# Optimization experiments

Hardware: AMD Instinct MI355X
Metric: run time of the kernel (lower is better)

Reference implementation:

```python
import jax, jax.numpy as jnp
import numpy as np

N_CLASSES = 12
IMG_SIZE = 512
BATCH = 8

CURV_MAX = jnp.array([1.2261, 1.1558, 1.1161, 1.1195, 2.7202, 2.3714,
                      1.7055, 3.2717, 2.6716, 5.0418, 0.4293], dtype=jnp.float32)


def setup_inputs() -> dict:
    key = jax.random.key(0)
    soft_anatomy = jax.random.normal(key, (BATCH, N_CLASSES, IMG_SIZE, IMG_SIZE), dtype=jnp.float32)
    return {"soft_anatomy": soft_anatomy}


def reference(soft_anatomy):
    nc1 = N_CLASSES - 1  # 11 layer channels
    pred_mask = soft_anatomy[:, :nc1]                      # [B, 11, H, W]
    sm = jax.nn.softmax(pred_mask, axis=2)                 # softmax over height (dim 2)
    lsm = jax.nn.log_softmax(pred_mask, axis=2)
    B, C, H, W = sm.shape

    # position mask: row index broadcast over width/channels
    pos = jnp.arange(H, dtype=sm.dtype)[None, None, :, None]  # [1,1,H,1]

    # expected layer position per column: [B, 11, W]
    layer_positions = jnp.sum(sm * pos, axis=2)

    # std deviations around layer positions: [B, 11, W]
    std_deviations = jnp.sqrt(
        jnp.sum(sm * (pos - layer_positions[:, :, None, :]) ** 2, axis=2))

    # topology violations between adjacent layers: [B, 10, W]
    topology_violations = jax.nn.relu(layer_positions[:, :-1] - layer_positions[:, 1:])

    # neighbour (continuity) diff along width: [B, 11, W-1]
    continuity_violations = jnp.abs(
        (jnp.roll(layer_positions, 1, axis=2) - layer_positions)[..., 1:])

    # curvature via depthwise conv1d with sobel [-1,0..0,1] and laplace [1,0..0,-2,0..0,1]
    # (kernel length 11, replicate pad 5 -> same width). torch conv1d is cross-correlation:
    #   first[w]  = -x[w] + x[w+10]
    #   second[w] =  x[w] - 2*x[w+5] + x[w+10]
    PAD = 5
    lpp = jnp.pad(layer_positions, ((0, 0), (0, 0), (PAD, PAD)), mode='edge')
    first_order = lpp[..., 10:] - lpp[..., :-10]
    second_order = lpp[..., :-10] - 2.0 * lpp[..., 5:-5] + lpp[..., 10:]
    curvature = second_order / jnp.power(1.0 + first_order ** 2, 1.5)
    curvature_diffs = jnp.abs(curvature) - CURV_MAX[None, :, None]  # curv_max broadcast over W

    # topological_engine_1d: new[i] = max(new[i-1], lp[i]) == cumulative max over class dim
    correct_layer_positions = jax.lax.cummax(layer_positions, axis=1)

    # cumulative mask: ones channel + cumsum over height -> [B, 12, H, W]
    cum = jnp.cumsum(sm, axis=2)
    ones = jnp.ones((B, 1, H, W), dtype=sm.dtype)
    cm = jnp.concatenate([ones, cum], axis=1)

    # topological_engine_2d: y[idx] = relu(c[idx] + y[idx-1] - 1), idx = 2..n_classes-1
    def step(carry, c):
        y = jax.nn.relu(c + carry - 1.0)
        return y, y

    _, ys = jax.lax.scan(step, cm[:, 1], jnp.moveaxis(cm[:, 2:], 1, 0))
    top_correct = jnp.concatenate([cm[:, :2], jnp.moveaxis(ys, 0, 1)], axis=1)  # [B,12,H,W]

    # separate_masks: forward diff in place; last channel unchanged
    clean_masks = jnp.concatenate(
        [top_correct[:, :-1] - top_correct[:, 1:], top_correct[:, -1:]], axis=1)

    return (lsm, correct_layer_positions, clean_masks,
            std_deviations, topology_violations, continuity_violations, curvature_diffs)
```

## Files before the change

kernel.cpp:

```cpp
#include <hip/hip_runtime.h>

#define BB 8
#define NC 12
#define NC1 11
#define HH 512
#define WW 512
#define NCH 32
#define HC 16
#define NBC (BB*NC1)

static constexpr size_t CH_STRIDE = (size_t)HH * WW;

static constexpr size_t OFF_LSM   = 0;
static constexpr size_t OFF_CLP   = 23068672;
static constexpr size_t OFF_CLEAN = 23113728;
static constexpr size_t OFF_STD   = 48279552;
static constexpr size_t OFF_TOPO  = 48324608;
static constexpr size_t OFF_CONT  = 48365568;
static constexpr size_t OFF_CURV  = 48410536;

static constexpr size_t WS_E    = 0;
static constexpr size_t WS_P    = (size_t)NBC * NCH * WW;
static constexpr size_t WS_Q    = 2 * WS_P;
static constexpr size_t WS_INVS = 3 * WS_P;
static constexpr size_t WS_LOGS = WS_INVS + (size_t)NBC * WW;
static constexpr size_t WS_LP   = WS_LOGS + (size_t)NBC * WW;

__global__ __launch_bounds__(512) void k1_partials(const float* __restrict__ in,
                                                   float* __restrict__ ws) {
    const int w = threadIdx.x;
    const int chunk = blockIdx.x;
    const int bc = blockIdx.y;
    const int b = bc / NC1, c = bc % NC1;

    const float* p = in + ((size_t)(b * NC + c) * HH + (size_t)chunk * HC) * WW + w;
    float E = 0.f, P = 0.f, Q = 0.f;
#pragma unroll
    for (int i = 0; i < HC; ++i) {
        float x = p[(size_t)i * WW];
        float e = expf(x);
        float h = (float)(chunk * HC + i);
        E += e;
        P += h * e;
        Q += h * h * e;
    }
    size_t o = ((size_t)bc * NCH + chunk) * WW + w;
    ws[WS_E + o] = E;
    ws[WS_P + o] = P;
    ws[WS_Q + o] = Q;
}

__global__ __launch_bounds__(512) void k2_reduce(float* __restrict__ ws,
                                                 float* __restrict__ out) {
    const int w = threadIdx.x;
    const int bc = blockIdx.x;

    const size_t base0 = (size_t)bc * NCH * WW + w;
    float Ee[NCH];
    double S = 0.0, P = 0.0, Q = 0.0;
#pragma unroll
    for (int k = 0; k < NCH; ++k) {
        float e = ws[WS_E + base0 + (size_t)k * WW];
        Ee[k] = e;
        S += (double)e;
        P += (double)ws[WS_P + base0 + (size_t)k * WW];
        Q += (double)ws[WS_Q + base0 + (size_t)k * WW];
    }
    const double inv = 1.0 / S;
    double pre = 0.0;
#pragma unroll
    for (int k = 0; k < NCH; ++k) {
        ws[WS_E + base0 + (size_t)k * WW] = (float)(pre * inv);
        pre += (double)Ee[k];
    }
    const double lp = P * inv;
    double var = Q * inv - lp * lp;
    if (var < 0.0) var = 0.0;

    const size_t o = (size_t)bc * WW + w;
    ws[WS_INVS + o] = (float)inv;
    ws[WS_LOGS + o] = (float)log(S);
    ws[WS_LP + o]   = (float)lp;
    out[OFF_STD + o] = (float)sqrt(var);
}

__global__ __launch_bounds__(512) void k3_small(const float* __restrict__ lp,
                                                float* __restrict__ out) {
    const int w = threadIdx.x;
    const int b = blockIdx.x;
    const float CM[NC1] = {1.2261f, 1.1558f, 1.1161f, 1.1195f, 2.7202f, 2.3714f,
                           1.7055f, 3.2717f, 2.6716f, 5.0418f, 0.4293f};
    float lpv[NC1];
#pragma unroll
    for (int c = 0; c < NC1; ++c)
        lpv[c] = lp[(size_t)(b * NC1 + c) * WW + w];

    float m = lpv[0];
#pragma unroll
    for (int c = 0; c < NC1; ++c) {
        m = fmaxf(m, lpv[c]);
        out[OFF_CLP + (size_t)(b * NC1 + c) * WW + w] = m;
    }
#pragma unroll
    for (int c = 0; c < NC1 - 1; ++c)
        out[OFF_TOPO + (size_t)(b * (NC1 - 1) + c) * WW + w] = fmaxf(lpv[c] - lpv[c + 1], 0.f);
    if (w < WW - 1) {
#pragma unroll
        for (int c = 0; c < NC1; ++c) {
            float nxt = lp[(size_t)(b * NC1 + c) * WW + w + 1];
            out[OFF_CONT + (size_t)(b * NC1 + c) * (WW - 1) + w] = fabsf(lpv[c] - nxt);
        }
    }
    const int wm = (w - 5 < 0) ? 0 : w - 5;
    const int wp = (w + 5 > WW - 1) ? WW - 1 : w + 5;
#pragma unroll
    for (int c = 0; c < NC1; ++c) {
        float a  = lp[(size_t)(b * NC1 + c) * WW + wm];
        float bb = lp[(size_t)(b * NC1 + c) * WW + wp];
        float fo = bb - a;
        float so = a - 2.f * lpv[c] + bb;
        float bs = 1.f + fo * fo;
        float cv = so / (bs * sqrtf(bs));
        out[OFF_CURV + (size_t)(b * NC1 + c) * WW + w] = fabsf(cv) - CM[c];
    }
}

__global__ __launch_bounds__(256) void k4_main(const float* __restrict__ in,
                                               const float* __restrict__ ws,
                                               float* __restrict__ out) {
    const int tid = threadIdx.x;
    const int whalf = blockIdx.x;
    const int chunk = blockIdx.y;
    const int b = blockIdx.z;
    const int w = whalf * 256 + tid;

    float cum[NC1], inv[NC1], lgs[NC1];
#pragma unroll
    for (int c = 0; c < NC1; ++c) {
        size_t bc = (size_t)(b * NC1 + c);
        cum[c] = ws[WS_E + (bc * NCH + chunk) * WW + w];
        inv[c] = ws[WS_INVS + bc * WW + w];
        lgs[c] = ws[WS_LOGS + bc * WW + w];
    }

    for (int i = 0; i < HC; ++i) {
        const int h = chunk * HC + i;
        float x[NC1];
#pragma unroll
        for (int c = 0; c < NC1; ++c)
            x[c] = in[(size_t)(b * NC + c) * CH_STRIDE + (size_t)h * WW + w];
#pragma unroll
        for (int c = 0; c < NC1; ++c) {
            cum[c] += expf(x[c]) * inv[c];
            out[OFF_LSM + (size_t)(b * NC1 + c) * CH_STRIDE + (size_t)h * WW + w] = x[c] - lgs[c];
        }
        const size_t ob = OFF_CLEAN + (size_t)(b * NC) * CH_STRIDE + (size_t)h * WW + w;
        float tc = cum[0];
        out[ob] = 1.f - tc;
#pragma unroll
        for (int k = 1; k < NC1; ++k) {
            float t2 = fmaxf(cum[k] + tc - 1.f, 0.f);
            out[ob + (size_t)k * CH_STRIDE] = tc - t2;
            tc = t2;
        }
        out[ob + (size_t)NC1 * CH_STRIDE] = tc;
    }
}

extern "C" void kernel_launch(void* const* d_in, const int* in_sizes, int n_in,
                              void* d_out, int out_size, void* d_ws, size_t ws_size,
                              hipStream_t stream) {
    const float* in = (const float*)d_in[0];
    float* out = (float*)d_out;
    float* ws = (float*)d_ws;

    hipLaunchKernelGGL(k1_partials, dim3(NCH, NBC), dim3(512), 0, stream, in, ws);
    hipLaunchKernelGGL(k2_reduce, dim3(NBC), dim3(512), 0, stream, ws, out);
    hipLaunchKernelGGL(k3_small, dim3(BB), dim3(512), 0, stream, ws + WS_LP, out);
    hipLaunchKernelGGL(k4_main, dim3(2, NCH, BB), dim3(256), 0, stream, in, ws, out);
}
```

Before: 75.84 us.

## Fuse stats passes into one block-reduced kernel and fold small outputs into emit

Replaces the four-kernel pipeline with two kernels. The first computes per-column exp sums, moments and the prefix sums of the softmax within one block through shared memory, so the partial P/Q round-trip through global memory and the separate reduce kernel are no longer needed. The second kernel emits log-softmax and the clean masks using float2 vector accesses with finer height groups, and its g==0 blocks also compute the small per-column outputs, which removes one more launch. The reductions now run in float instead of double, which may slightly change precision, and the first kernel launches only 352 blocks, each walking the full height.

```diff
diff --git a/kernel.cpp b/kernel.cpp
--- a/kernel.cpp
+++ b/kernel.cpp
@@ -5,165 +5,167 @@
 #define NC1 11
 #define HH 512
 #define WW 512
-#define NCH 32
-#define HC 16
-#define NBC (BB*NC1)
+#define NG 64
+#define GH 8
 
-static constexpr size_t CH_STRIDE = (size_t)HH * WW;
+static constexpr size_t CH = (size_t)HH * WW;
 
 static constexpr size_t OFF_LSM   = 0;
-static constexpr size_t OFF_CLP   = 23068672;
-static constexpr size_t OFF_CLEAN = 23113728;
-static constexpr size_t OFF_STD   = 48279552;
-static constexpr size_t OFF_TOPO  = 48324608;
-static constexpr size_t OFF_CONT  = 48365568;
-static constexpr size_t OFF_CURV  = 48410536;
+static constexpr size_t OFF_CLP   = (size_t)BB * NC1 * CH;
+static constexpr size_t OFF_CLEAN = OFF_CLP + (size_t)BB * NC1 * WW;
+static constexpr size_t OFF_STD   = OFF_CLEAN + (size_t)BB * NC * CH;
+static constexpr size_t OFF_TOPO  = OFF_STD + (size_t)BB * NC1 * WW;
+static constexpr size_t OFF_CONT  = OFF_TOPO + (size_t)BB * (NC1 - 1) * WW;
+static constexpr size_t OFF_CURV  = OFF_CONT + (size_t)BB * NC1 * (WW - 1);
 
-static constexpr size_t WS_E    = 0;
-static constexpr size_t WS_P    = (size_t)NBC * NCH * WW;
-static constexpr size_t WS_Q    = 2 * WS_P;
-static constexpr size_t WS_INVS = 3 * WS_P;
-static constexpr size_t WS_LOGS = WS_INVS + (size_t)NBC * WW;
-static constexpr size_t WS_LP   = WS_LOGS + (size_t)NBC * WW;
+static constexpr size_t WS_BASE = 0;
+static constexpr size_t WS_INV  = WS_BASE + (size_t)BB * NC1 * NG * WW;
+static constexpr size_t WS_LOG  = WS_INV + (size_t)BB * NC1 * WW;
+static constexpr size_t WS_LP   = WS_LOG + (size_t)BB * NC1 * WW;
 
-__global__ __launch_bounds__(512) void k1_partials(const float* __restrict__ in,
-                                                   float* __restrict__ ws) {
-    const int w = threadIdx.x;
-    const int chunk = blockIdx.x;
-    const int bc = blockIdx.y;
-    const int b = bc / NC1, c = bc % NC1;
+__global__ __launch_bounds__(256) void ka_stats(const float* __restrict__ in,
+                                                float* __restrict__ ws,
+                                                float* __restrict__ out) {
+    const int tx = threadIdx.x & 63;
+    const int ty = threadIdx.x >> 6;
+    const int wt = blockIdx.x;
+    const int c  = blockIdx.y;
+    const int b  = blockIdx.z;
+    const int w  = wt * 128 + tx * 2;
+    const int bc = b * NC1 + c;
 
-    const float* p = in + ((size_t)(b * NC + c) * HH + (size_t)chunk * HC) * WW + w;
-    float E = 0.f, P = 0.f, Q = 0.f;
+    __shared__ float lE[NG][128];
+    __shared__ float lP[4][128];
+    __shared__ float lQ[4][128];
+
+    const float* p = in + (size_t)(b * NC + c) * CH + (size_t)(ty * 128) * WW + w;
+    float Px = 0.f, Py = 0.f, Qx = 0.f, Qy = 0.f;
+    for (int gl = 0; gl < 16; ++gl) {
+        float Ex = 0.f, Ey = 0.f, P8x = 0.f, P8y = 0.f, Q8x = 0.f, Q8y = 0.f;
+        const float hbase = (float)(ty * 128 + gl * 8);
 #pragma unroll
-    for (int i = 0; i < HC; ++i) {
-        float x = p[(size_t)i * WW];
-        float e = expf(x);
-        float h = (float)(chunk * HC + i);
-        E += e;
-        P += h * e;
-        Q += h * h * e;
+        for (int i = 0; i < GH; ++i) {
+            float2 x = *(const float2*)(p + (size_t)(gl * 8 + i) * WW);
+            float ex = expf(x.x), ey = expf(x.y);
+            float h = hbase + (float)i;
+            Ex += ex; Ey += ey;
+            P8x += h * ex; P8y += h * ey;
+            Q8x += h * h * ex; Q8y += h * h * ey;
+        }
+        *(float2*)&lE[ty * 16 + gl][tx * 2] = make_float2(Ex, Ey);
+        Px += P8x; Py += P8y;
+        Qx += Q8x; Qy += Q8y;
     }
-    size_t o = ((size_t)bc * NCH + chunk) * WW + w;
-    ws[WS_E + o] = E;
-    ws[WS_P + o] = P;
-    ws[WS_Q + o] = Q;
+    *(float2*)&lP[ty][tx * 2] = make_float2(Px, Py);
+    *(float2*)&lQ[ty][tx * 2] = make_float2(Qx, Qy);
+    __syncthreads();
+    if (ty != 0) return;
+
+    float Sx = 0.f, Sy = 0.f;
+#pragma unroll
+    for (int g = 0; g < NG; ++g) {
+        float2 e = *(const float2*)&lE[g][tx * 2];
+        Sx += e.x; Sy += e.y;
+    }
+    const float invx = 1.f / Sx, invy = 1.f / Sy;
+    float rx = 0.f, ry = 0.f;
+    float* bp = ws + WS_BASE + (size_t)bc * NG * WW + w;
+#pragma unroll
+    for (int g = 0; g < NG; ++g) {
+        *(float2*)(bp + (size_t)g * WW) = make_float2(rx * invx, ry * invy);
+        float2 e = *(const float2*)&lE[g][tx * 2];
+        rx += e.x; ry += e.y;
+    }
+    float Ptx = lP[0][tx*2] + lP[1][tx*2] + lP[2][tx*2] + lP[3][tx*2];
+    float Pty = lP[0][tx*2+1] + lP[1][tx*2+1] + lP[2][tx*2+1] + lP[3][tx*2+1];
+    float Qtx = lQ[0][tx*2] + lQ[1][tx*2] + lQ[2][tx*2] + lQ[3][tx*2];
+    float Qty = lQ[0][tx*2+1] + lQ[1][tx*2+1] + lQ[2][tx*2+1] + lQ[3][tx*2+1];
+    float lpx = Ptx * invx, lpy = Pty * invy;
+    float vx = Qtx * invx - lpx * lpx; if (vx < 0.f) vx = 0.f;
+    float vy = Qty * invy - lpy * lpy; if (vy < 0.f) vy = 0.f;
+
+    const size_t o = (size_t)bc * WW + w;
+    *(float2*)(ws + WS_INV + o) = make_float2(invx, invy);
+    *(float2*)(ws + WS_LOG + o) = make_float2(logf(Sx), logf(Sy));
+    *(float2*)(ws + WS_LP + o)  = make_float2(lpx, lpy);
+    *(float2*)(out + OFF_STD + o) = make_float2(sqrtf(vx), sqrtf(vy));
 }
 
-__global__ __launch_bounds__(512) void k2_reduce(float* __restrict__ ws,
-                                                 float* __restrict__ out) {
-    const int w = threadIdx.x;
-    const int bc = blockIdx.x;
+__global__ __launch_bounds__(256) void kb_emit(const float* __restrict__ in,
+                                               const float* __restrict__ ws,
+                                               float* __restrict__ out) {
+    const int t = threadIdx.x;
+    const int g = blockIdx.x;
+    const int b = blockIdx.y;
+    const int w = t * 2;
 
-    const size_t base0 = (size_t)bc * NCH * WW + w;
-    float Ee[NCH];
-    double S = 0.0, P = 0.0, Q = 0.0;
+    float2 cum[NC1], inv[NC1], lgs[NC1];
 #pragma unroll
-    for (int k = 0; k < NCH; ++k) {
-        float e = ws[WS_E + base0 + (size_t)k * WW];
-        Ee[k] = e;
-        S += (double)e;
-        P += (double)ws[WS_P + base0 + (size_t)k * WW];
-        Q += (double)ws[WS_Q + base0 + (size_t)k * WW];
+    for (int c = 0; c < NC1; ++c) {
+        const size_t bc = (size_t)(b * NC1 + c);
+        cum[c] = *(const float2*)(ws + WS_BASE + (bc * NG + g) * WW + w);
+        inv[c] = *(const float2*)(ws + WS_INV + bc * WW + w);
+        lgs[c] = *(const float2*)(ws + WS_LOG + bc * WW + w);
     }
-    const double inv = 1.0 / S;
-    double pre = 0.0;
+    const float* ip  = in + (size_t)b * NC * CH + (size_t)(g * GH) * WW + w;
+    float* lsm = out + OFF_LSM + (size_t)b * NC1 * CH + (size_t)(g * GH) * WW + w;
+    float* cln = out + OFF_CLEAN + (size_t)b * NC * CH + (size_t)(g * GH) * WW + w;
+
+    for (int i = 0; i < GH; ++i) {
+        const size_t ho = (size_t)i * WW;
+        float2 x[NC1];
 #pragma unroll
-    for (int k = 0; k < NCH; ++k) {
-        ws[WS_E + base0 + (size_t)k * WW] = (float)(pre * inv);
-        pre += (double)Ee[k];
+        for (int c = 0; c < NC1; ++c)
+            x[c] = *(const float2*)(ip + (size_t)c * CH + ho);
+#pragma unroll
+        for (int c = 0; c < NC1; ++c) {
+            cum[c].x += expf(x[c].x) * inv[c].x;
+            cum[c].y += expf(x[c].y) * inv[c].y;
+            *(float2*)(lsm + (size_t)c * CH + ho) =
+                make_float2(x[c].x - lgs[c].x, x[c].y - lgs[c].y);
+        }
+        float2 tc = cum[0];
+        *(float2*)(cln + ho) = make_float2(1.f - tc.x, 1.f - tc.y);
+#pragma unroll
+        for (int k = 1; k < NC1; ++k) {
+            float2 t2 = make_float2(fmaxf(cum[k].x + tc.x - 1.f, 0.f),
+                                    fmaxf(cum[k].y + tc.y - 1.f, 0.f));
+            *(float2*)(cln + (size_t)k * CH + ho) = make_float2(tc.x - t2.x, tc.y - t2.y);
+            tc = t2;
+        }
+        *(float2*)(cln + (size_t)NC1 * CH + ho) = tc;
     }
-    const double lp = P * inv;
-    double var = Q * inv - lp * lp;
-    if (var < 0.0) var = 0.0;
 
-    const size_t o = (size_t)bc * WW + w;
-    ws[WS_INVS + o] = (float)inv;
-    ws[WS_LOGS + o] = (float)log(S);
-    ws[WS_LP + o]   = (float)lp;
-    out[OFF_STD + o] = (float)sqrt(var);
-}
-
-__global__ __launch_bounds__(512) void k3_small(const float* __restrict__ lp,
-                                                float* __restrict__ out) {
-    const int w = threadIdx.x;
-    const int b = blockIdx.x;
+    if (g != 0) return;
     const float CM[NC1] = {1.2261f, 1.1558f, 1.1161f, 1.1195f, 2.7202f, 2.3714f,
                            1.7055f, 3.2717f, 2.6716f, 5.0418f, 0.4293f};
-    float lpv[NC1];
+    const float* lp = ws + WS_LP;
 #pragma unroll
-    for (int c = 0; c < NC1; ++c)
-        lpv[c] = lp[(size_t)(b * NC1 + c) * WW + w];
-
-    float m = lpv[0];
-#pragma unroll
-    for (int c = 0; c < NC1; ++c) {
-        m = fmaxf(m, lpv[c]);
-        out[OFF_CLP + (size_t)(b * NC1 + c) * WW + w] = m;
-    }
-#pragma unroll
-    for (int c = 0; c < NC1 - 1; ++c)
-        out[OFF_TOPO + (size_t)(b * (NC1 - 1) + c) * WW + w] = fmaxf(lpv[c] - lpv[c + 1], 0.f);
-    if (w < WW - 1) {
-#pragma unroll
+    for (int s = 0; s < 2; ++s) {
+        const int wv = w + s;
+        const int wm = (wv - 5 < 0) ? 0 : wv - 5;
+        const int wp = (wv + 5 > WW - 1) ? WW - 1 : wv + 5;
+        float m = 0.f, prev = 0.f;
         for (int c = 0; c < NC1; ++c) {
-            float nxt = lp[(size_t)(b * NC1 + c) * WW + w + 1];
-            out[OFF_CONT + (size_t)(b * NC1 + c) * (WW - 1) + w] = fabsf(lpv[c] - nxt);
+            const size_t rb = (size_t)(b * NC1 + c) * WW;
+            const float lv = lp[rb + wv];
+            m = (c == 0) ? lv : fmaxf(m, lv);
+            out[OFF_CLP + rb + wv] = m;
+            if (c > 0)
+                out[OFF_TOPO + (size_t)(b * (NC1 - 1) + (c - 1)) * WW + wv] =
+                    fmaxf(prev - lv, 0.f);
+            prev = lv;
+            if (wv < WW - 1) {
+                const float nxt = lp[rb + wv + 1];
+                out[OFF_CONT + (size_t)(b * NC1 + c) * (WW - 1) + wv] = fabsf(lv - nxt);
+            }
+            const float a  = lp[rb + wm];
+            const float bb = lp[rb + wp];
+            const float fo = bb - a;
+            const float so = a - 2.f * lv + bb;
+            const float bs = 1.f + fo * fo;
+            out[OFF_CURV + rb + wv] = fabsf(so / (bs * sqrtf(bs))) - CM[c];
         }
-    }
-    const int wm = (w - 5 < 0) ? 0 : w - 5;
-    const int wp = (w + 5 > WW - 1) ? WW - 1 : w + 5;
-#pragma unroll
-    for (int c = 0; c < NC1; ++c) {
-        float a  = lp[(size_t)(b * NC1 + c) * WW + wm];
-        float bb = lp[(size_t)(b * NC1 + c) * WW + wp];
-        float fo = bb - a;
-        float so = a - 2.f * lpv[c] + bb;
-        float bs = 1.f + fo * fo;
-        float cv = so / (bs * sqrtf(bs));
-        out[OFF_CURV + (size_t)(b * NC1 + c) * WW + w] = fabsf(cv) - CM[c];
-    }
-}
-
-__global__ __launch_bounds__(256) void k4_main(const float* __restrict__ in,
-                                               const float* __restrict__ ws,
-                                               float* __restrict__ out) {
-    const int tid = threadIdx.x;
-    const int whalf = blockIdx.x;
-    const int chunk = blockIdx.y;
-    const int b = blockIdx.z;
-    const int w = whalf * 256 + tid;
-
-    float cum[NC1], inv[NC1], lgs[NC1];
-#pragma unroll
-    for (int c = 0; c < NC1; ++c) {
-        size_t bc = (size_t)(b * NC1 + c);
-        cum[c] = ws[WS_E + (bc * NCH + chunk) * WW + w];
-        inv[c] = ws[WS_INVS + bc * WW + w];
-        lgs[c] = ws[WS_LOGS + bc * WW + w];
-    }
-
-    for (int i = 0; i < HC; ++i) {
-        const int h = chunk * HC + i;
-        float x[NC1];
-#pragma unroll
-        for (int c = 0; c < NC1; ++c)
-            x[c] = in[(size_t)(b * NC + c) * CH_STRIDE + (size_t)h * WW + w];
-#pragma unroll
-        for (int c = 0; c < NC1; ++c) {
-            cum[c] += expf(x[c]) * inv[c];
-            out[OFF_LSM + (size_t)(b * NC1 + c) * CH_STRIDE + (size_t)h * WW + w] = x[c] - lgs[c];
-        }
-        const size_t ob = OFF_CLEAN + (size_t)(b * NC) * CH_STRIDE + (size_t)h * WW + w;
-        float tc = cum[0];
-        out[ob] = 1.f - tc;
-#pragma unroll
-        for (int k = 1; k < NC1; ++k) {
-            float t2 = fmaxf(cum[k] + tc - 1.f, 0.f);
-            out[ob + (size_t)k * CH_STRIDE] = tc - t2;
-            tc = t2;
-        }
-        out[ob + (size_t)NC1 * CH_STRIDE] = tc;
     }
 }
 
@@ -174,8 +176,6 @@
     float* out = (float*)d_out;
     float* ws = (float*)d_ws;
 
-    hipLaunchKernelGGL(k1_partials, dim3(NCH, NBC), dim3(512), 0, stream, in, ws);
-    hipLaunchKernelGGL(k2_reduce, dim3(NBC), dim3(512), 0, stream, ws, out);
-    hipLaunchKernelGGL(k3_small, dim3(BB), dim3(512), 0, stream, ws + WS_LP, out);
-    hipLaunchKernelGGL(k4_main, dim3(2, NCH, BB), dim3(256), 0, stream, in, ws, out);
+    hipLaunchKernelGGL(ka_stats, dim3(4, NC1, BB), dim3(256), 0, stream, in, ws, out);
+    hipLaunchKernelGGL(kb_emit, dim3(NG, BB), dim3(256), 0, stream, in, ws, out);
 }
```

After: 83.54 us. +10.2%, slower.
